# Kernel tuning notes

Hardware: AMD Instinct MI355X
Metric: run time of the kernel (lower is better)

The kernel has to match this reference:

```python
import jax, jax.numpy as jnp
import numpy as np

T, IN, H, OUT = 4096, 1024, 1024, 512


def setup_inputs() -> dict:
    key = jax.random.key(0)
    ks = jax.random.split(key, 7)
    s_g = 1.0 / np.sqrt(H + IN)  # xavier-ish scale for gate weights
    s_y = 1.0 / np.sqrt(H)
    return {
        "x": jax.random.normal(ks[0], (T, IN), jnp.float32),
        "wf": jax.random.normal(ks[1], (H, H + IN), jnp.float32) * s_g,
        "bf": jnp.zeros((H,), jnp.float32),
        "wi": jax.random.normal(ks[2], (H, H + IN), jnp.float32) * s_g,
        "bi": jnp.zeros((H,), jnp.float32),
        "wc": jax.random.normal(ks[3], (H, H + IN), jnp.float32) * s_g,
        "bc": jnp.zeros((H,), jnp.float32),
        "wo": jax.random.normal(ks[4], (H, H + IN), jnp.float32) * s_g,
        "bo": jnp.zeros((H,), jnp.float32),
        "why": jax.random.normal(ks[5], (OUT, H), jnp.float32) * s_y,
        "by": jnp.zeros((OUT,), jnp.float32),
    }


def reference(x, wf, bf, wi, bi, wc, bc, wo, bo, why, by):
    hid = wf.shape[0]

    def step(carry, x_t):
        h, c = carry
        concat = jnp.concatenate([h, x_t])  # (H+IN,)
        f = jax.nn.sigmoid(wf @ concat + bf)
        i = jax.nn.sigmoid(wi @ concat + bi)
        o = jax.nn.sigmoid(wo @ concat + bo)
        g = jnp.tanh(wc @ concat + bc)
        c_new = f * c + i * g
        h_new = o * jnp.tanh(c_new)
        y = why @ h_new + by  # (OUT,)
        return (h_new, c_new), y

    h0 = jnp.zeros((hid,), x.dtype)
    c0 = jnp.zeros((hid,), x.dtype)
    (h, c), ys = jax.lax.scan(step, (h0, c0), x)
    return ys, h, c
```

## Files before the change

kernel.cpp:

```cpp
#include <hip/hip_runtime.h>
#include <stdint.h>

#define TT 4096
#define INW 1024
#define HW 1024
#define OUTW 512
#define CH 2048


__device__ __forceinline__ uint64_t pack_pair(float v, uint32_t ep) {
    return ((uint64_t)ep << 32) | (uint64_t)__float_as_uint(v);
}
__device__ __forceinline__ float sigmoid_fast(float z) {
    return 1.0f / (1.0f + __expf(-z));
}
__device__ __forceinline__ float tanh_fast(float z) {
    return 1.0f - 2.0f / (1.0f + __expf(2.0f * z));
}

template <int CTRL>
__device__ __forceinline__ float dpp_add(float v) {
    int s = __builtin_amdgcn_update_dpp(0, __float_as_int(v), CTRL, 0xF, 0xF, true);
    return v + __int_as_float(s);
}
__device__ __forceinline__ float wave_sum_to_lane63(float v) {
    v = dpp_add<0x111>(v);
    v = dpp_add<0x112>(v);
    v = dpp_add<0x114>(v);
    v = dpp_add<0x118>(v);
    v = dpp_add<0x142>(v);
    v = dpp_add<0x143>(v);
    return v;
}

__global__ void lstm_init_kernel(uint64_t* __restrict__ hpair) {
    int j = blockIdx.x * blockDim.x + threadIdx.x;
    if (j < HW) {
        hpair[j]      = pack_pair(0.0f, 0u);
        hpair[HW + j] = pack_pair(0.0f, 0x80000000u);
    }
}

__global__ __launch_bounds__(256, 1) void lstm_seq_kernel(
    const float* __restrict__ x,
    const float* __restrict__ wf, const float* __restrict__ bf,
    const float* __restrict__ wi, const float* __restrict__ bi,
    const float* __restrict__ wc, const float* __restrict__ bc,
    const float* __restrict__ wo, const float* __restrict__ bo,
    uint64_t* __restrict__ hpair, float* __restrict__ h_all,
    float* __restrict__ out)
{
    __shared__ float hsh[2][HW];

    const int tid  = threadIdx.x;
    const int lane = tid & 63;
    const int w    = tid >> 6;
    const int b    = blockIdx.x;
    const int gu   = b * 4 + w;

    float wh[64], wx[64];
    {
        const float* wptr[4] = {wf, wi, wc, wo};
#pragma unroll
        for (int g = 0; g < 4; ++g) {
            const float* base = wptr[g] + (size_t)gu * CH + lane;
#pragma unroll
            for (int k = 0; k < 16; ++k) wh[g * 16 + k] = base[(size_t)k * 64];
#pragma unroll
            for (int k = 0; k < 16; ++k) wx[g * 16 + k] = base[1024 + (size_t)k * 64];
        }
    }
#pragma unroll
    for (int i = 0; i < 64; ++i) {
        asm volatile("" : "+v"(wh[i]));
        asm volatile("" : "+v"(wx[i]));
    }

    const float bias0 = bf[gu];
    const float bias1 = bi[gu];
    const float bias2 = bc[gu];
    const float bias3 = bo[gu];

    float xacc0 = 0.f, xacc1 = 0.f, xacc2 = 0.f, xacc3 = 0.f;
    {
        const float* xp = x + lane;
        float xv[16];
#pragma unroll
        for (int k = 0; k < 16; ++k) xv[k] = xp[(size_t)k * 64];
#pragma unroll
        for (int k = 0; k < 16; ++k) {
            xacc0 = fmaf(wx[0 * 16 + k], xv[k], xacc0);
            xacc1 = fmaf(wx[1 * 16 + k], xv[k], xacc1);
            xacc2 = fmaf(wx[2 * 16 + k], xv[k], xacc2);
            xacc3 = fmaf(wx[3 * 16 + k], xv[k], xacc3);
        }
    }

    float c = 0.0f, h_last = 0.0f;

    for (int t = 0; t < TT; ++t) {
        const int p = t & 1;

        const uint64_t* hp = hpair + (size_t)p * HW + 256 * w + lane;
        float hq[4];
        {
            bool ok;
            do {
                uint64_t pv[4];
#pragma unroll
                for (int k = 0; k < 4; ++k)
                    pv[k] = __hip_atomic_load(&hp[64 * k],
                                              __ATOMIC_RELAXED, __HIP_MEMORY_SCOPE_SYSTEM);
                ok = true;
#pragma unroll
                for (int k = 0; k < 4; ++k)
                    ok &= ((uint32_t)(pv[k] >> 32) == (uint32_t)t);
#pragma unroll
                for (int k = 0; k < 4; ++k)
                    hq[k] = __uint_as_float((uint32_t)pv[k]);
            } while (!__all(ok));
        }

#pragma unroll
        for (int k = 0; k < 4; ++k)
            hsh[p][256 * w + lane + 64 * k] = hq[k];
        __syncthreads();

        float xn[16];
        {
            const int tn = (t + 1 < TT) ? t + 1 : t;
            const float* xp = x + (size_t)tn * INW + lane;
#pragma unroll
            for (int k = 0; k < 16; ++k) xn[k] = xp[(size_t)k * 64];
        }

        if (t >= 1 && b == (t & 255)) {
            float4 hv4 = *(const float4*)&hsh[p][tid * 4];
            *(float4*)(h_all + (size_t)(t - 1) * HW + tid * 4) = hv4;
        }

        float acc0 = xacc0, acc1 = xacc1, acc2 = xacc2, acc3 = xacc3;
#pragma unroll
        for (int k = 0; k < 16; ++k) {
            float v = hsh[p][lane + 64 * k];
            acc0 = fmaf(wh[0 * 16 + k], v, acc0);
            acc1 = fmaf(wh[1 * 16 + k], v, acc1);
            acc2 = fmaf(wh[2 * 16 + k], v, acc2);
            acc3 = fmaf(wh[3 * 16 + k], v, acc3);
        }

        acc0 = wave_sum_to_lane63(acc0);
        acc1 = wave_sum_to_lane63(acc1);
        acc2 = wave_sum_to_lane63(acc2);
        acc3 = wave_sum_to_lane63(acc3);

        if (lane == 63) {
            float f  = sigmoid_fast(acc0 + bias0);
            float ii = sigmoid_fast(acc1 + bias1);
            float g  = tanh_fast(acc2 + bias2);
            float o  = sigmoid_fast(acc3 + bias3);
            c = fmaf(f, c, ii * g);
            float hn = o * tanh_fast(c);
            h_last = hn;
            __hip_atomic_store(&hpair[(size_t)((t + 1) & 1) * HW + gu],
                               pack_pair(hn, (uint32_t)(t + 1)),
                               __ATOMIC_RELAXED, __HIP_MEMORY_SCOPE_SYSTEM);
        }
        __builtin_amdgcn_sched_barrier(0);

        float nx0 = 0.f, nx1 = 0.f, nx2 = 0.f, nx3 = 0.f;
#pragma unroll
        for (int k = 0; k < 16; ++k) {
            nx0 = fmaf(wx[0 * 16 + k], xn[k], nx0);
            nx1 = fmaf(wx[1 * 16 + k], xn[k], nx1);
            nx2 = fmaf(wx[2 * 16 + k], xn[k], nx2);
            nx3 = fmaf(wx[3 * 16 + k], xn[k], nx3);
        }
        xacc0 = nx0; xacc1 = nx1; xacc2 = nx2; xacc3 = nx3;
    }

    if (lane == 63) {
        h_all[(size_t)(TT - 1) * HW + gu] = h_last;
        out[(size_t)TT * OUTW + gu]      = h_last;
        out[(size_t)TT * OUTW + HW + gu] = c;
    }
}

__global__ __launch_bounds__(256) void lstm_ygemm_kernel(
    const float* __restrict__ hall, const float* __restrict__ why,
    const float* __restrict__ by, float* __restrict__ ys)
{
    __shared__ float hs[64][17];
    __shared__ float wsm[64][17];
    const int t0 = blockIdx.x * 64, o0 = blockIdx.y * 64;
    const int tid = threadIdx.x;
    const int tx = tid & 15, ty = tid >> 4;

    float acc[4][4] = {};
    const int r = tid >> 2;
    const int cc = (tid & 3) * 4;

    for (int kk = 0; kk < HW; kk += 16) {
        float4 hv = *(const float4*)(hall + (size_t)(t0 + r) * HW + kk + cc);
        hs[r][cc + 0] = hv.x; hs[r][cc + 1] = hv.y;
        hs[r][cc + 2] = hv.z; hs[r][cc + 3] = hv.w;
        float4 wv = *(const float4*)(why + (size_t)(o0 + r) * HW + kk + cc);
        wsm[r][cc + 0] = wv.x; wsm[r][cc + 1] = wv.y;
        wsm[r][cc + 2] = wv.z; wsm[r][cc + 3] = wv.w;
        __syncthreads();
#pragma unroll
        for (int k = 0; k < 16; ++k) {
            float ha[4], wa[4];
#pragma unroll
            for (int i = 0; i < 4; ++i) ha[i] = hs[ty * 4 + i][k];
#pragma unroll
            for (int j = 0; j < 4; ++j) wa[j] = wsm[tx * 4 + j][k];
#pragma unroll
            for (int i = 0; i < 4; ++i)
#pragma unroll
                for (int j = 0; j < 4; ++j)
                    acc[i][j] = fmaf(ha[i], wa[j], acc[i][j]);
        }
        __syncthreads();
    }
#pragma unroll
    for (int i = 0; i < 4; ++i) {
#pragma unroll
        for (int j = 0; j < 4; ++j) {
            int oo = o0 + tx * 4 + j;
            ys[(size_t)(t0 + ty * 4 + i) * OUTW + oo] = acc[i][j] + by[oo];
        }
    }
}

extern "C" void kernel_launch(void* const* d_in, const int* in_sizes, int n_in,
                              void* d_out, int out_size, void* d_ws, size_t ws_size,
                              hipStream_t stream) {
    const float* x   = (const float*)d_in[0];
    const float* wf  = (const float*)d_in[1];
    const float* bf  = (const float*)d_in[2];
    const float* wi  = (const float*)d_in[3];
    const float* bi  = (const float*)d_in[4];
    const float* wc  = (const float*)d_in[5];
    const float* bc  = (const float*)d_in[6];
    const float* wo  = (const float*)d_in[7];
    const float* bo  = (const float*)d_in[8];
    const float* why = (const float*)d_in[9];
    const float* by  = (const float*)d_in[10];
    float* out = (float*)d_out;

    uint64_t* hpair = (uint64_t*)d_ws;
    float* h_all = (float*)((char*)d_ws + (size_t)2 * HW * sizeof(uint64_t));

    lstm_init_kernel<<<dim3(4), dim3(256), 0, stream>>>(hpair);
    lstm_seq_kernel<<<dim3(256), dim3(256), 0, stream>>>(
        x, wf, bf, wi, bi, wc, bc, wo, bo, hpair, h_all, out);
    lstm_ygemm_kernel<<<dim3(64, 8), dim3(256), 0, stream>>>(h_all, why, by, out);
}
```

Before: 6.757 ms.

## Pipeline polling loads and replace block barrier with LDS flag spin

The spin-wait on the global h/epoch pairs now keeps two probe sets in flight, issuing the next load before checking the previous one, and the first probe for the next step is issued right after the cell update. The per-step __syncthreads is replaced by per-wave LDS flags that each wave spins on. The x prefetch is moved after the gate computation. This aims to shorten the critical-path latency of the cross-block handoff each timestep, at the cost of extra memory traffic from speculative polling and reliance on LDS ordering through manual waitcnt.

```diff
diff --git a/kernel.cpp b/kernel.cpp
--- a/kernel.cpp
+++ b/kernel.cpp
@@ -40,6 +40,18 @@
         hpair[HW + j] = pack_pair(0.0f, 0x80000000u);
     }
 }
+
+#define PROBE(d0, d1, d2, d3, base)                                                   \
+    do {                                                                              \
+        d0 = __hip_atomic_load((base),       __ATOMIC_RELAXED, __HIP_MEMORY_SCOPE_SYSTEM); \
+        d1 = __hip_atomic_load((base) + 64,  __ATOMIC_RELAXED, __HIP_MEMORY_SCOPE_SYSTEM); \
+        d2 = __hip_atomic_load((base) + 128, __ATOMIC_RELAXED, __HIP_MEMORY_SCOPE_SYSTEM); \
+        d3 = __hip_atomic_load((base) + 192, __ATOMIC_RELAXED, __HIP_MEMORY_SCOPE_SYSTEM); \
+    } while (0)
+
+#define EPOCH_HIT(d0, d1, d2, d3, ep)                                  \
+    __all(((uint32_t)((d0) >> 32) == (ep)) & ((uint32_t)((d1) >> 32) == (ep)) & \
+          ((uint32_t)((d2) >> 32) == (ep)) & ((uint32_t)((d3) >> 32) == (ep)))
 
 __global__ __launch_bounds__(256, 1) void lstm_seq_kernel(
     const float* __restrict__ x,
@@ -51,6 +63,7 @@
     float* __restrict__ out)
 {
     __shared__ float hsh[2][HW];
+    __shared__ int   flg[2][4];
 
     const int tid  = threadIdx.x;
     const int lane = tid & 63;
@@ -58,6 +71,8 @@
     const int b    = blockIdx.x;
     const int gu   = b * 4 + w;
 
+    if (tid < 8) flg[tid >> 2][tid & 3] = -1;
+
     float wh[64], wx[64];
     {
         const float* wptr[4] = {wf, wi, wc, wo};
@@ -96,43 +111,55 @@
         }
     }
 
+    __syncthreads();
+
     float c = 0.0f, h_last = 0.0f;
+
+    uint64_t pa0, pa1, pa2, pa3, pb0, pb1, pb2, pb3;
+    PROBE(pa0, pa1, pa2, pa3, hpair + 256 * w + lane);
 
     for (int t = 0; t < TT; ++t) {
         const int p = t & 1;
-
         const uint64_t* hp = hpair + (size_t)p * HW + 256 * w + lane;
-        float hq[4];
-        {
-            bool ok;
-            do {
-                uint64_t pv[4];
-#pragma unroll
-                for (int k = 0; k < 4; ++k)
-                    pv[k] = __hip_atomic_load(&hp[64 * k],
-                                              __ATOMIC_RELAXED, __HIP_MEMORY_SCOPE_SYSTEM);
-                ok = true;
-#pragma unroll
-                for (int k = 0; k < 4; ++k)
-                    ok &= ((uint32_t)(pv[k] >> 32) == (uint32_t)t);
-#pragma unroll
-                for (int k = 0; k < 4; ++k)
-                    hq[k] = __uint_as_float((uint32_t)pv[k]);
-            } while (!__all(ok));
-        }
-
-#pragma unroll
-        for (int k = 0; k < 4; ++k)
-            hsh[p][256 * w + lane + 64 * k] = hq[k];
-        __syncthreads();
-
-        float xn[16];
-        {
-            const int tn = (t + 1 < TT) ? t + 1 : t;
-            const float* xp = x + (size_t)tn * INW + lane;
-#pragma unroll
-            for (int k = 0; k < 16; ++k) xn[k] = xp[(size_t)k * 64];
-        }
+        const uint32_t ep = (uint32_t)t;
+
+        float hq0, hq1, hq2, hq3;
+        for (;;) {
+            PROBE(pb0, pb1, pb2, pb3, hp);
+            __builtin_amdgcn_sched_barrier(0);
+            if (EPOCH_HIT(pa0, pa1, pa2, pa3, ep)) {
+                hq0 = __uint_as_float((uint32_t)pa0);
+                hq1 = __uint_as_float((uint32_t)pa1);
+                hq2 = __uint_as_float((uint32_t)pa2);
+                hq3 = __uint_as_float((uint32_t)pa3);
+                break;
+            }
+            PROBE(pa0, pa1, pa2, pa3, hp);
+            __builtin_amdgcn_sched_barrier(0);
+            if (EPOCH_HIT(pb0, pb1, pb2, pb3, ep)) {
+                hq0 = __uint_as_float((uint32_t)pb0);
+                hq1 = __uint_as_float((uint32_t)pb1);
+                hq2 = __uint_as_float((uint32_t)pb2);
+                hq3 = __uint_as_float((uint32_t)pb3);
+                break;
+            }
+        }
+
+        hsh[p][256 * w + lane]       = hq0;
+        hsh[p][256 * w + lane + 64]  = hq1;
+        hsh[p][256 * w + lane + 128] = hq2;
+        hsh[p][256 * w + lane + 192] = hq3;
+        asm volatile("s_waitcnt lgkmcnt(0)" ::: "memory");
+        if (lane == 0)
+            __hip_atomic_store(&flg[p][w], t, __ATOMIC_RELAXED, __HIP_MEMORY_SCOPE_WORKGROUP);
+        for (;;) {
+            int f0 = __hip_atomic_load(&flg[p][0], __ATOMIC_RELAXED, __HIP_MEMORY_SCOPE_WORKGROUP);
+            int f1 = __hip_atomic_load(&flg[p][1], __ATOMIC_RELAXED, __HIP_MEMORY_SCOPE_WORKGROUP);
+            int f2 = __hip_atomic_load(&flg[p][2], __ATOMIC_RELAXED, __HIP_MEMORY_SCOPE_WORKGROUP);
+            int f3 = __hip_atomic_load(&flg[p][3], __ATOMIC_RELAXED, __HIP_MEMORY_SCOPE_WORKGROUP);
+            if (((f0 ^ t) | (f1 ^ t) | (f2 ^ t) | (f3 ^ t)) == 0) break;
+        }
+        __builtin_amdgcn_sched_barrier(0);
 
         if (t >= 1 && b == (t & 255)) {
             float4 hv4 = *(const float4*)&hsh[p][tid * 4];
@@ -168,6 +195,15 @@
         }
         __builtin_amdgcn_sched_barrier(0);
 
+        PROBE(pa0, pa1, pa2, pa3, hpair + (size_t)((t + 1) & 1) * HW + 256 * w + lane);
+
+        float xn[16];
+        {
+            const int tn = (t + 1 < TT) ? t + 1 : t;
+            const float* xp = x + (size_t)tn * INW + lane;
+#pragma unroll
+            for (int k = 0; k < 16; ++k) xn[k] = xp[(size_t)k * 64];
+        }
         float nx0 = 0.f, nx1 = 0.f, nx2 = 0.f, nx3 = 0.f;
 #pragma unroll
         for (int k = 0; k < 16; ++k) {
```

Result: slower. 18.46 ms (+173.1%).

## Assign two hidden units per wave and halve the persistent LSTM grid

Applied to the files above, without the earlier changes.

Each wave now computes two hidden units, so the grid shrinks from 256 to 128 blocks and weights held in registers double to 256 floats per lane. Both new h values are published with one 16-byte store carrying value/epoch pairs, issued through inline asm with sc0 sc1 cache bits. The goal is fewer blocks taking part in the per-step global spin-wait and fewer store transactions. The cost is heavy register pressure (possible spills at 256 VGPRs plus temporaries) and twice the serial FMA and reduction work per wave on each step.

```diff
diff --git a/kernel.cpp b/kernel.cpp
--- a/kernel.cpp
+++ b/kernel.cpp
@@ -7,6 +7,8 @@
 #define OUTW 512
 #define CH 2048
 
+
+typedef uint32_t u32x4 __attribute__((ext_vector_type(4)));
 
 __device__ __forceinline__ uint64_t pack_pair(float v, uint32_t ep) {
     return ((uint64_t)ep << 32) | (uint64_t)__float_as_uint(v);
@@ -56,32 +58,39 @@
     const int lane = tid & 63;
     const int w    = tid >> 6;
     const int b    = blockIdx.x;
-    const int gu   = b * 4 + w;
-
-    float wh[64], wx[64];
+    const int gu0  = b * 8 + 2 * w;
+
+    float wh[128], wx[128];
     {
         const float* wptr[4] = {wf, wi, wc, wo};
 #pragma unroll
-        for (int g = 0; g < 4; ++g) {
-            const float* base = wptr[g] + (size_t)gu * CH + lane;
-#pragma unroll
-            for (int k = 0; k < 16; ++k) wh[g * 16 + k] = base[(size_t)k * 64];
-#pragma unroll
-            for (int k = 0; k < 16; ++k) wx[g * 16 + k] = base[1024 + (size_t)k * 64];
-        }
-    }
-#pragma unroll
-    for (int i = 0; i < 64; ++i) {
+        for (int u = 0; u < 2; ++u) {
+#pragma unroll
+            for (int g = 0; g < 4; ++g) {
+                const float* base = wptr[g] + (size_t)(gu0 + u) * CH + lane;
+#pragma unroll
+                for (int k = 0; k < 16; ++k) wh[u * 64 + g * 16 + k] = base[(size_t)k * 64];
+#pragma unroll
+                for (int k = 0; k < 16; ++k) wx[u * 64 + g * 16 + k] = base[1024 + (size_t)k * 64];
+            }
+        }
+    }
+#pragma unroll
+    for (int i = 0; i < 128; ++i) {
         asm volatile("" : "+v"(wh[i]));
         asm volatile("" : "+v"(wx[i]));
     }
 
-    const float bias0 = bf[gu];
-    const float bias1 = bi[gu];
-    const float bias2 = bc[gu];
-    const float bias3 = bo[gu];
-
-    float xacc0 = 0.f, xacc1 = 0.f, xacc2 = 0.f, xacc3 = 0.f;
+    float bias[8];
+#pragma unroll
+    for (int u = 0; u < 2; ++u) {
+        bias[u * 4 + 0] = bf[gu0 + u];
+        bias[u * 4 + 1] = bi[gu0 + u];
+        bias[u * 4 + 2] = bc[gu0 + u];
+        bias[u * 4 + 3] = bo[gu0 + u];
+    }
+
+    float xacc[8] = {0.f, 0.f, 0.f, 0.f, 0.f, 0.f, 0.f, 0.f};
     {
         const float* xp = x + lane;
         float xv[16];
@@ -89,14 +98,13 @@
         for (int k = 0; k < 16; ++k) xv[k] = xp[(size_t)k * 64];
 #pragma unroll
         for (int k = 0; k < 16; ++k) {
-            xacc0 = fmaf(wx[0 * 16 + k], xv[k], xacc0);
-            xacc1 = fmaf(wx[1 * 16 + k], xv[k], xacc1);
-            xacc2 = fmaf(wx[2 * 16 + k], xv[k], xacc2);
-            xacc3 = fmaf(wx[3 * 16 + k], xv[k], xacc3);
-        }
-    }
-
-    float c = 0.0f, h_last = 0.0f;
+#pragma unroll
+            for (int j = 0; j < 8; ++j)
+                xacc[j] = fmaf(wx[(j >> 2) * 64 + (j & 3) * 16 + k], xv[k], xacc[j]);
+        }
+    }
+
+    float c0 = 0.f, c1 = 0.f, h0_last = 0.f, h1_last = 0.f;
 
     for (int t = 0; t < TT; ++t) {
         const int p = t & 1;
@@ -134,55 +142,67 @@
             for (int k = 0; k < 16; ++k) xn[k] = xp[(size_t)k * 64];
         }
 
-        if (t >= 1 && b == (t & 255)) {
+        if (t >= 1 && b == (t & 127)) {
             float4 hv4 = *(const float4*)&hsh[p][tid * 4];
             *(float4*)(h_all + (size_t)(t - 1) * HW + tid * 4) = hv4;
         }
 
-        float acc0 = xacc0, acc1 = xacc1, acc2 = xacc2, acc3 = xacc3;
+        float acc[8];
+#pragma unroll
+        for (int j = 0; j < 8; ++j) acc[j] = xacc[j];
 #pragma unroll
         for (int k = 0; k < 16; ++k) {
             float v = hsh[p][lane + 64 * k];
-            acc0 = fmaf(wh[0 * 16 + k], v, acc0);
-            acc1 = fmaf(wh[1 * 16 + k], v, acc1);
-            acc2 = fmaf(wh[2 * 16 + k], v, acc2);
-            acc3 = fmaf(wh[3 * 16 + k], v, acc3);
-        }
-
-        acc0 = wave_sum_to_lane63(acc0);
-        acc1 = wave_sum_to_lane63(acc1);
-        acc2 = wave_sum_to_lane63(acc2);
-        acc3 = wave_sum_to_lane63(acc3);
+#pragma unroll
+            for (int j = 0; j < 8; ++j)
+                acc[j] = fmaf(wh[(j >> 2) * 64 + (j & 3) * 16 + k], v, acc[j]);
+        }
+
+#pragma unroll
+        for (int j = 0; j < 8; ++j) acc[j] = wave_sum_to_lane63(acc[j]);
 
         if (lane == 63) {
-            float f  = sigmoid_fast(acc0 + bias0);
-            float ii = sigmoid_fast(acc1 + bias1);
-            float g  = tanh_fast(acc2 + bias2);
-            float o  = sigmoid_fast(acc3 + bias3);
-            c = fmaf(f, c, ii * g);
-            float hn = o * tanh_fast(c);
-            h_last = hn;
-            __hip_atomic_store(&hpair[(size_t)((t + 1) & 1) * HW + gu],
-                               pack_pair(hn, (uint32_t)(t + 1)),
-                               __ATOMIC_RELAXED, __HIP_MEMORY_SCOPE_SYSTEM);
+            float f0  = sigmoid_fast(acc[0] + bias[0]);
+            float i0  = sigmoid_fast(acc[1] + bias[1]);
+            float g0  = tanh_fast(acc[2] + bias[2]);
+            float o0  = sigmoid_fast(acc[3] + bias[3]);
+            c0 = fmaf(f0, c0, i0 * g0);
+            float hn0 = o0 * tanh_fast(c0);
+            float f1  = sigmoid_fast(acc[4] + bias[4]);
+            float i1  = sigmoid_fast(acc[5] + bias[5]);
+            float g1  = tanh_fast(acc[6] + bias[6]);
+            float o1  = sigmoid_fast(acc[7] + bias[7]);
+            c1 = fmaf(f1, c1, i1 * g1);
+            float hn1 = o1 * tanh_fast(c1);
+            h0_last = hn0; h1_last = hn1;
+            const uint32_t ep1 = (uint32_t)(t + 1);
+            u32x4 st;
+            st.x = __float_as_uint(hn0); st.y = ep1;
+            st.z = __float_as_uint(hn1); st.w = ep1;
+            uint64_t* dst = hpair + (size_t)((t + 1) & 1) * HW + gu0;
+            asm volatile("global_store_dwordx4 %0, %1, off sc0 sc1"
+                         :: "v"((void*)dst), "v"(st) : "memory");
         }
         __builtin_amdgcn_sched_barrier(0);
 
-        float nx0 = 0.f, nx1 = 0.f, nx2 = 0.f, nx3 = 0.f;
-#pragma unroll
-        for (int k = 0; k < 16; ++k) {
-            nx0 = fmaf(wx[0 * 16 + k], xn[k], nx0);
-            nx1 = fmaf(wx[1 * 16 + k], xn[k], nx1);
-            nx2 = fmaf(wx[2 * 16 + k], xn[k], nx2);
-            nx3 = fmaf(wx[3 * 16 + k], xn[k], nx3);
-        }
-        xacc0 = nx0; xacc1 = nx1; xacc2 = nx2; xacc3 = nx3;
+        float nx[8] = {0.f, 0.f, 0.f, 0.f, 0.f, 0.f, 0.f, 0.f};
+#pragma unroll
+        for (int k = 0; k < 16; ++k) {
+#pragma unroll
+            for (int j = 0; j < 8; ++j)
+                nx[j] = fmaf(wx[(j >> 2) * 64 + (j & 3) * 16 + k], xn[k], nx[j]);
+        }
+#pragma unroll
+        for (int j = 0; j < 8; ++j) xacc[j] = nx[j];
     }
 
     if (lane == 63) {
-        h_all[(size_t)(TT - 1) * HW + gu] = h_last;
-        out[(size_t)TT * OUTW + gu]      = h_last;
-        out[(size_t)TT * OUTW + HW + gu] = c;
+        h_all[(size_t)(TT - 1) * HW + gu0]     = h0_last;
+        h_all[(size_t)(TT - 1) * HW + gu0 + 1] = h1_last;
+        out[(size_t)TT * OUTW + gu0]           = h0_last;
+        out[(size_t)TT * OUTW + gu0 + 1]       = h1_last;
+        out[(size_t)TT * OUTW + HW + gu0]      = c0;
+        out[(size_t)TT * OUTW + HW + gu0 + 1]  = c1;
     }
 }
 
@@ -253,7 +273,7 @@
     float* h_all = (float*)((char*)d_ws + (size_t)2 * HW * sizeof(uint64_t));
 
     lstm_init_kernel<<<dim3(4), dim3(256), 0, stream>>>(hpair);
-    lstm_seq_kernel<<<dim3(256), dim3(256), 0, stream>>>(
+    lstm_seq_kernel<<<dim3(128), dim3(256), 0, stream>>>(
         x, wf, bf, wi, bi, wc, bc, wo, bo, hpair, h_all, out);
     lstm_ygemm_kernel<<<dim3(64, 8), dim3(256), 0, stream>>>(h_all, why, by, out);
 }
```

Measured after the change: 10.74 ms. 58.9% more time.
